# Kernel tuning notes

Hardware: AMD Instinct MI355X
Metric: run time of the kernel (lower is better)

Reference implementation:

```python
import jax, jax.numpy as jnp
import numpy as np

# ---- module config (init_kwargs) ----
B, CIN, H, W_ = 2, 64, 56, 56
COUT, KH, KW = 128, 3, 3
K = CIN * KH * KW               # 576, reduction dim
ARRAY_ROWS = 128
IN_SLICES = (2, 2, 2, 2)        # 8-bit inputs, 2-bit slices
W_SLICES = (2, 2, 2, 2)         # 8-bit weights, 2-bit slices
N_STEPS_IN = 2 ** sum(IN_SLICES)    # 256, unsigned quantizer
N_STEPS_W = 2 ** sum(W_SLICES)      # 256
ADC_BINS = 256
ADC_STEP = 4.0

def _shifts_masks(slices):
    masks, shifts = [], [0]
    for s in slices[::-1]:
        masks.append((1 << s) - 1)
        shifts.append(s + shifts[-1])
    return np.array(shifts[-2::-1], np.int32), np.array(masks[::-1], np.int32)

_ish, _im = _shifts_masks(IN_SLICES)
_wsh, _wm = _shifts_masks(W_SLICES)
ISH, IM = jnp.asarray(_ish), jnp.asarray(_im)
WSH, WM = jnp.asarray(_wsh), jnp.asarray(_wm)
ISF = jnp.asarray((1 << _ish).astype(np.float32))  # slice recombine weights 2^shift
WSF = jnp.asarray((1 << _wsh).astype(np.float32))


def setup_inputs() -> dict:
    key = jax.random.key(0)
    k1, k2 = jax.random.split(key)
    return {
        "x": jax.random.normal(k1, (B, CIN, H, W_), jnp.float32),
        "w": jax.random.normal(k2, (COUT, CIN, KH, KW), jnp.float32),
    }


def _im2col(x):
    # 3x3 SAME conv patches, ordering [Cin, kh, kw] to match w.reshape(COUT, K)
    xp = jnp.pad(x, ((0, 0), (0, 0), (1, 1), (1, 1)))
    cols = jnp.stack([xp[:, :, i:i + H, j:j + W_]
                      for i in range(KH) for j in range(KW)], axis=2)  # [B,Cin,9,H,W]
    return cols.transpose(0, 3, 4, 1, 2).reshape(B * H * W_, K)  # [Nx, K]


def _quant_unsigned(v, n_steps):
    # Quantizer.offset + Quantizer.forward (unsigned, per-row over dim=-1)
    offs = v.min(axis=-1, keepdims=True)
    vr = v - offs
    step = vr.max(axis=-1, keepdims=True) / (n_steps - 1)
    q = jnp.round(jnp.clip(vr, 0.0, step * n_steps) / step).astype(jnp.int32)
    return q, step[..., 0], offs[..., 0]


def _slice_bits(q, shifts, masks):
    # Slicer.forward: stack (q >> shift) & mask along new leading slice dim
    s = shifts.reshape((-1,) + (1,) * q.ndim)
    m = masks.reshape((-1,) + (1,) * q.ndim)
    return (q[None] >> s) & m


def _chunk(t):
    # Chunker.forward over last dim K
    nb = -(-K // ARRAY_ROWS)
    npb = -(-K // nb)
    pad = nb * npb - K
    t = jnp.pad(t, [(0, 0)] * (t.ndim - 1) + [(0, pad)])
    t = t.reshape(t.shape[:-1] + (nb, npb))
    return jnp.moveaxis(t, -2, 0)  # [nb, ..., npb]


def reference(x, w):
    xf = _im2col(x)                    # [Nx, K]
    wf = w.reshape(COUT, K)            # [Ny, K]
    x_sum = xf.sum(axis=-1)            # [Nx]
    w_sum = wf.sum(axis=-1)            # [Ny]

    xq, x_scale, x_offs = _quant_unsigned(xf, N_STEPS_IN)
    wq, w_scale, w_offs = _quant_unsigned(wf, N_STEPS_W)

    xc = _chunk(_slice_bits(xq, ISH, IM))  # [nb, nis, Nx, npb] int32
    wc = _chunk(_slice_bits(wq, WSH, WM))  # [nb, nws, Ny, npb] int32

    # bit-serial crossbar MACs per (chunk, weight-slice, input-slice)
    z = jnp.einsum('bixk,bwyk->bwixy',
                   xc.astype(jnp.float32), wc.astype(jnp.float32))  # [nb,nws,nis,Nx,Ny]

    # ADC digitization (unsigned, fixed step): quantize then dequantize
    z = jnp.round(jnp.clip(z, 0.0, ADC_STEP * ADC_BINS) / ADC_STEP) * ADC_STEP

    # Chunker.reverse: sum crossbar blocks; Slicer.reverse: shift-weighted sums
    z = z.sum(axis=0)                               # [nws,nis,Nx,Ny]
    z = jnp.einsum('wixy,w,i->xy', z, WSF, ISF)     # [Nx,Ny]

    # dequantize scales and unsigned-offset correction:
    # x.y = sx*sy*(xq.yq) + x_offs*sum(y) + y_offs*sum(x) - x_offs*y_offs*K
    z = z * x_scale[:, None] * w_scale[None, :]
    z = (z + x_offs[:, None] * w_sum[None, :]
           + w_offs[None, :] * x_sum[:, None]
           - x_offs[:, None] * w_offs[None, :] * K)

    return z.reshape(B, H, W_, COUT).transpose(0, 3, 1, 2)  # [B,Cout,H,W]
```

## Files before the change

kernel.cpp:

```cpp
#include <hip/hip_runtime.h>


#define NY    128
#define KDIM  576
#define NCH   5
#define NPB   116

typedef int i32x4 __attribute__((ext_vector_type(4)));
typedef float f32x4 __attribute__((ext_vector_type(4)));

extern __shared__ unsigned char lds[];

__device__ __forceinline__ i32x4 slice2b(i32x4 v, int sh) {
    i32x4 r;
    r[0] = (int)(((unsigned)v[0] >> sh) & 0x03030303u);
    r[1] = (int)(((unsigned)v[1] >> sh) & 0x03030303u);
    r[2] = (int)(((unsigned)v[2] >> sh) & 0x03030303u);
    r[3] = (int)(((unsigned)v[3] >> sh) & 0x03030303u);
    return r;
}

__device__ __forceinline__ void quant36(const float (&v)[36], unsigned char* rowp,
                                        int i16, float* sc_s, float* of_s,
                                        float* sm_s, int sidx)
{
    float mn = v[0], mx = v[0], sm = 0.f;
#pragma unroll
    for (int m = 0; m < 36; m++) { mn = fminf(mn, v[m]); mx = fmaxf(mx, v[m]); sm += v[m]; }
#pragma unroll
    for (int off = 1; off < 16; off <<= 1) {
        mn = fminf(mn, __shfl_xor(mn, off));
        mx = fmaxf(mx, __shfl_xor(mx, off));
        sm += __shfl_xor(sm, off);
    }
    float step = (mx - mn) / 255.0f;
    if (i16 == 0) { sc_s[sidx] = step; of_s[sidx] = mn; sm_s[sidx] = sm; }
    int k0 = i16 * 36;
#pragma unroll
    for (int d = 0; d < 9; d++) {
        unsigned int dw = 0;
#pragma unroll
        for (int mb = 0; mb < 4; mb++) {
            int q = (int)rintf((v[d * 4 + mb] - mn) / step);
            q = q < 0 ? 0 : (q > 255 ? 255 : q);
            dw |= (unsigned)q << (8 * mb);
        }
        int kd = k0 + d * 4;
        int ch = kd / NPB;
        *(unsigned int*)(rowp + kd + 12 * ch) = dw;
    }
}

__global__ __launch_bounds__(1024) void k_all(
    const float* __restrict__ x, const float* __restrict__ w,
    float* __restrict__ out)
{
    unsigned char* stgW = lds;
    unsigned char* stgX = lds + 81920;
    float* xsc = (float*)(lds + 102400);
    float* xof = xsc + 32;  float* xsm = xof + 32;
    float* wsc = xsm + 32;  float* wof = wsc + 128;  float* wsm = wof + 128;
    unsigned char* scr = lds + 104320;
    float* xs2 = (float*)(lds + 125312);

    int tid = threadIdx.x, wv = tid >> 6, lane = tid & 63;
    int g = lane >> 4, i16 = lane & 15;
    int blk = blockIdx.x;
    int b = blk >= 98 ? 1 : 0;
    int pos_base = (blk - 98 * b) * 32;
    const float* xb = x + (size_t)(b * 64) * 3136;

    for (int i = tid; i < 64 * 102; i += 1024) {
        int cin = i / 102, rem = i - cin * 102;
        int kh = rem / 34;
        int gg = pos_base + (rem - kh * 34) - 1;
        float vv = 0.f;
        if (gg >= 0 && gg < 3136) {
            int hg = gg / 56, wg = gg - hg * 56;
            int r = hg - 1 + kh;
            if (r >= 0 && r < 56) vv = xb[cin * 3136 + r * 56 + wg];
        }
        xs2[cin * 103 + rem] = vv;
    }
    if (tid < 512) {
        int tile = tid >> 8, rl = (tid >> 4) & 15, dwp = tid & 15;
        int col = dwp < 12 ? (dwp / 3) * 128 + 116 + (dwp % 3) * 4
                           : 624 + (dwp - 12) * 4;
        *(unsigned int*)(scr + tile * 10496 + rl * 656 + col) = 0u;
    }
    __syncthreads();

    if (wv < 8) {
        int i = wv * 4 + g;
        int pos = pos_base + i;
        int w_ = pos - (pos / 56) * 56;
        float v[36];
#pragma unroll
        for (int m = 0; m < 36; m++) {
            int r9 = m % 9, kh = r9 / 3, kw = r9 - kh * 3;
            int cin = i16 * 4 + m / 9;
            int ww = w_ - 1 + kw;
            v[m] = (ww >= 0 && ww < 56) ? xs2[cin * 103 + kh * 34 + i + kw] : 0.f;
        }
        quant36(v, scr + (i >> 4) * 10496 + (i & 15) * 656, i16, xsc, xof, xsm, i);
    }
    __syncthreads();

    for (int idx = tid; idx < 2 * 640; idx += 1024) {
        int tile = idx / 640, rr = idx - tile * 640;
        int u = rr >> 4, rl = rr & 15;
        *(i32x4*)(stgX + tile * 10240 + rr * 16) =
            *(const i32x4*)(scr + tile * 10496 + rl * 656 + u * 16);
    }
    __syncthreads();

    {
        int tile = tid >> 8, rl = (tid >> 4) & 15, dwp = tid & 15;
        int col = dwp < 12 ? (dwp / 3) * 128 + 116 + (dwp % 3) * 4
                           : 624 + (dwp - 12) * 4;
        *(unsigned int*)(scr + tile * 10496 + rl * 656 + col) = 0u;
    }
    {
        int row = wv * 4 + g;
        const float* wr = w + (size_t)row * KDIM + i16 * 36;
        float v[36];
#pragma unroll
        for (int d = 0; d < 9; d++) {
            f32x4 t = *(const f32x4*)(wr + d * 4);
            v[d*4+0] = t[0]; v[d*4+1] = t[1]; v[d*4+2] = t[2]; v[d*4+3] = t[3];
        }
        quant36(v, scr + (row >> 4) * 10496 + (row & 15) * 656, i16, wsc, wof, wsm, row);
    }
    __syncthreads();

    for (int idx = tid; idx < 4 * 640; idx += 1024) {
        int tile = idx / 640, rr = idx - tile * 640;
        int u = rr >> 4, rl = rr & 15;
        *(i32x4*)(stgW + tile * 10240 + rr * 16) =
            *(const i32x4*)(scr + tile * 10496 + rl * 656 + u * 16);
    }
    __syncthreads();

    {
        int row = 64 + wv * 4 + g;
        const float* wr = w + (size_t)row * KDIM + i16 * 36;
        float v[36];
#pragma unroll
        for (int d = 0; d < 9; d++) {
            f32x4 t = *(const f32x4*)(wr + d * 4);
            v[d*4+0] = t[0]; v[d*4+1] = t[1]; v[d*4+2] = t[2]; v[d*4+3] = t[3];
        }
        quant36(v, scr + ((row - 64) >> 4) * 10496 + (row & 15) * 656, i16, wsc, wof, wsm, row);
    }
    __syncthreads();

    for (int idx = tid; idx < 4 * 640; idx += 1024) {
        int tile = idx / 640, rr = idx - tile * 640;
        int u = rr >> 4, rl = rr & 15;
        *(i32x4*)(stgW + (4 + tile) * 10240 + rr * 16) =
            *(const i32x4*)(scr + tile * 10496 + rl * 656 + u * 16);
    }
    __syncthreads();

    int rt = wv >> 3, ctl = wv & 7;
    const unsigned char* Wb = stgW + ctl * 10240;
    const unsigned char* Xb = stgX + rt * 10240;

    i32x4 acc = {0, 0, 0, 0};
    const i32x4 zero = {0, 0, 0, 0};

    for (int chunk = 0; chunk < NCH; chunk++) {
        const i32x4* Ax = (const i32x4*)(Xb + chunk * 2048 + lane * 16);
        const i32x4* Aw = (const i32x4*)(Wb + chunk * 2048 + lane * 16);
        i32x4 ar0 = Ax[0], ar1 = Ax[64];
        i32x4 br0 = Aw[0], br1 = Aw[64];

        i32x4 ws_sl[4][2];
#pragma unroll
        for (int ws = 0; ws < 4; ws++) {
            ws_sl[ws][0] = slice2b(br0, 6 - 2 * ws);
            ws_sl[ws][1] = slice2b(br1, 6 - 2 * ws);
        }
#pragma unroll
        for (int is = 0; is < 4; is++) {
            int ish = 6 - 2 * is;
            i32x4 b0 = slice2b(ar0, ish);
            i32x4 b1 = slice2b(ar1, ish);
#pragma unroll
            for (int ws = 0; ws < 4; ws++) {
                i32x4 d = __builtin_amdgcn_mfma_i32_16x16x64_i8(ws_sl[ws][0], b0, zero, 0, 0, 0);
                d = __builtin_amdgcn_mfma_i32_16x16x64_i8(ws_sl[ws][1], b1, d, 0, 0, 0);
                int sh = ish + (6 - 2 * ws);
#pragma unroll
                for (int r = 0; r < 4; r++) {
                    int z = d[r];
                    z = z > 1024 ? 1024 : z;
                    int r4 = (z + 1 + ((z >> 2) & 1)) & ~3;
                    acc[r] += r4 << sh;
                }
            }
        }
    }

    int i_loc = rt * 16 + i16;
    float xs = xsc[i_loc], xo = xof[i_loc], xsmv = xsm[i_loc];
    int hw = pos_base + i_loc;
#pragma unroll
    for (int r = 0; r < 4; r++) {
        int wrow = ctl * 16 + g * 4 + r;
        float tt = ((float)acc[r] * xs) * wsc[wrow];
        float res = ((tt + xo * wsm[wrow]) + wof[wrow] * xsmv)
                  - (xo * wof[wrow]) * 576.0f;
        out[(b * 128 + wrow) * 3136 + hw] = res;
    }
}

extern "C" void kernel_launch(void* const* d_in, const int* in_sizes, int n_in,
                              void* d_out, int out_size, void* d_ws, size_t ws_size,
                              hipStream_t stream) {
    const float* x = (const float*)d_in[0];
    const float* w = (const float*)d_in[1];
    float* out = (float*)d_out;

    (void)hipFuncSetAttribute((const void*)k_all,
                              hipFuncAttributeMaxDynamicSharedMemorySize, 151680);

    hipLaunchKernelGGL(k_all, dim3(196), dim3(1024), 151680, stream, x, w, out);
}
```

Measured before the change: 41.19 us.

## Split weight quantization into separate kernel and shrink main tiles

Weight quantization moves out of every main-kernel block into a small prologue kernel that writes pre-quantized, MFMA-ordered weights plus their scales to workspace. The main kernel now uses 256-thread blocks over 16 positions and half of the output channels (784 blocks), and reads weight fragments straight from global memory. This removes the 196-fold redundant weight quantization and the large LDS footprint, raising occupancy. In exchange it adds a second launch and global-memory weight loads inside the MFMA loop, and recomputes the x halo tile twice per position tile.

```diff
diff --git a/kernel.cpp b/kernel.cpp
--- a/kernel.cpp
+++ b/kernel.cpp
@@ -1,15 +1,12 @@
 #include <hip/hip_runtime.h>
 
 
-#define NY    128
 #define KDIM  576
-#define NCH   5
 #define NPB   116
+#define SSTR  688
 
 typedef int i32x4 __attribute__((ext_vector_type(4)));
 typedef float f32x4 __attribute__((ext_vector_type(4)));
-
-extern __shared__ unsigned char lds[];
 
 __device__ __forceinline__ i32x4 slice2b(i32x4 v, int sh) {
     i32x4 r;
@@ -21,8 +18,8 @@
 }
 
 __device__ __forceinline__ void quant36(const float (&v)[36], unsigned char* rowp,
-                                        int i16, float* sc_s, float* of_s,
-                                        float* sm_s, int sidx)
+                                        int i16, float* sc, float* of,
+                                        float* sm_, int sidx)
 {
     float mn = v[0], mx = v[0], sm = 0.f;
 #pragma unroll
@@ -34,7 +31,7 @@
         sm += __shfl_xor(sm, off);
     }
     float step = (mx - mn) / 255.0f;
-    if (i16 == 0) { sc_s[sidx] = step; of_s[sidx] = mn; sm_s[sidx] = sm; }
+    if (i16 == 0) { sc[sidx] = step; of[sidx] = mn; sm_[sidx] = sm; }
     int k0 = i16 * 36;
 #pragma unroll
     for (int d = 0; d < 9; d++) {
@@ -51,48 +48,77 @@
     }
 }
 
-__global__ __launch_bounds__(1024) void k_all(
-    const float* __restrict__ x, const float* __restrict__ w,
-    float* __restrict__ out)
+__device__ __forceinline__ void zero_pads(unsigned char* scr, int tid) {
+    int rl = tid >> 4, dwp = tid & 15;
+    int col = dwp < 12 ? (dwp / 3) * 128 + 116 + (dwp % 3) * 4
+                       : 624 + (dwp - 12) * 4;
+    *(unsigned int*)(scr + rl * SSTR + col) = 0u;
+}
+
+__global__ __launch_bounds__(256) void k_wq(
+    const float* __restrict__ w, unsigned char* __restrict__ Wq,
+    float* __restrict__ wsc, float* __restrict__ wof, float* __restrict__ wsm)
 {
-    unsigned char* stgW = lds;
-    unsigned char* stgX = lds + 81920;
-    float* xsc = (float*)(lds + 102400);
-    float* xof = xsc + 32;  float* xsm = xof + 32;
-    float* wsc = xsm + 32;  float* wof = wsc + 128;  float* wsm = wof + 128;
-    unsigned char* scr = lds + 104320;
-    float* xs2 = (float*)(lds + 125312);
+    __shared__ __align__(16) unsigned char scrW[16 * SSTR];
+    int tid = threadIdx.x, wv = tid >> 6, lane = tid & 63;
+    int g = lane >> 4, i16 = lane & 15;
+    int ctile = blockIdx.x;
+
+    zero_pads(scrW, tid);
+    __syncthreads();
+
+    int rl = wv * 4 + g;
+    int row = ctile * 16 + rl;
+    const float* wr = w + (size_t)row * KDIM + i16 * 36;
+    float v[36];
+#pragma unroll
+    for (int d = 0; d < 9; d++) {
+        f32x4 t = *(const f32x4*)(wr + d * 4);
+        v[d*4+0] = t[0]; v[d*4+1] = t[1]; v[d*4+2] = t[2]; v[d*4+3] = t[3];
+    }
+    quant36(v, scrW + rl * SSTR, i16, wsc, wof, wsm, row);
+    __syncthreads();
+
+    for (int idx = tid; idx < 640; idx += 256)
+        *(i32x4*)(Wq + (size_t)ctile * 10240 + idx * 16) =
+            *(const i32x4*)(scrW + (idx & 15) * SSTR + (idx >> 4) * 16);
+}
+
+__global__ __launch_bounds__(256) void k_main(
+    const float* __restrict__ x, const unsigned char* __restrict__ Wq,
+    const float* __restrict__ wscg, const float* __restrict__ wofg,
+    const float* __restrict__ wsmg, float* __restrict__ out)
+{
+    __shared__ float xs2[64 * 57];
+    __shared__ __align__(16) unsigned char scrX[16 * SSTR];
+    __shared__ float xsc[16], xof[16], xsm[16];
 
     int tid = threadIdx.x, wv = tid >> 6, lane = tid & 63;
     int g = lane >> 4, i16 = lane & 15;
     int blk = blockIdx.x;
-    int b = blk >= 98 ? 1 : 0;
-    int pos_base = (blk - 98 * b) * 32;
+    int rtile = blk >> 1, chalf = blk & 1;
+    int b = rtile >= 196 ? 1 : 0;
+    int pos0 = (rtile - 196 * b) * 16;
     const float* xb = x + (size_t)(b * 64) * 3136;
 
-    for (int i = tid; i < 64 * 102; i += 1024) {
-        int cin = i / 102, rem = i - cin * 102;
-        int kh = rem / 34;
-        int gg = pos_base + (rem - kh * 34) - 1;
+    for (int i = tid; i < 64 * 54; i += 256) {
+        int cin = i / 54, rem = i - cin * 54;
+        int kh = rem / 18;
+        int gg = pos0 + (rem - kh * 18) - 1;
         float vv = 0.f;
         if (gg >= 0 && gg < 3136) {
             int hg = gg / 56, wg = gg - hg * 56;
             int r = hg - 1 + kh;
             if (r >= 0 && r < 56) vv = xb[cin * 3136 + r * 56 + wg];
         }
-        xs2[cin * 103 + rem] = vv;
-    }
-    if (tid < 512) {
-        int tile = tid >> 8, rl = (tid >> 4) & 15, dwp = tid & 15;
-        int col = dwp < 12 ? (dwp / 3) * 128 + 116 + (dwp % 3) * 4
-                           : 624 + (dwp - 12) * 4;
-        *(unsigned int*)(scr + tile * 10496 + rl * 656 + col) = 0u;
-    }
-    __syncthreads();
-
-    if (wv < 8) {
+        xs2[cin * 57 + rem] = vv;
+    }
+    zero_pads(scrX, tid);
+    __syncthreads();
+
+    {
         int i = wv * 4 + g;
-        int pos = pos_base + i;
+        int pos = pos0 + i;
         int w_ = pos - (pos / 56) * 56;
         float v[36];
 #pragma unroll
@@ -100,86 +126,30 @@
             int r9 = m % 9, kh = r9 / 3, kw = r9 - kh * 3;
             int cin = i16 * 4 + m / 9;
             int ww = w_ - 1 + kw;
-            v[m] = (ww >= 0 && ww < 56) ? xs2[cin * 103 + kh * 34 + i + kw] : 0.f;
-        }
-        quant36(v, scr + (i >> 4) * 10496 + (i & 15) * 656, i16, xsc, xof, xsm, i);
-    }
-    __syncthreads();
-
-    for (int idx = tid; idx < 2 * 640; idx += 1024) {
-        int tile = idx / 640, rr = idx - tile * 640;
-        int u = rr >> 4, rl = rr & 15;
-        *(i32x4*)(stgX + tile * 10240 + rr * 16) =
-            *(const i32x4*)(scr + tile * 10496 + rl * 656 + u * 16);
-    }
-    __syncthreads();
-
-    {
-        int tile = tid >> 8, rl = (tid >> 4) & 15, dwp = tid & 15;
-        int col = dwp < 12 ? (dwp / 3) * 128 + 116 + (dwp % 3) * 4
-                           : 624 + (dwp - 12) * 4;
-        *(unsigned int*)(scr + tile * 10496 + rl * 656 + col) = 0u;
-    }
-    {
-        int row = wv * 4 + g;
-        const float* wr = w + (size_t)row * KDIM + i16 * 36;
-        float v[36];
-#pragma unroll
-        for (int d = 0; d < 9; d++) {
-            f32x4 t = *(const f32x4*)(wr + d * 4);
-            v[d*4+0] = t[0]; v[d*4+1] = t[1]; v[d*4+2] = t[2]; v[d*4+3] = t[3];
-        }
-        quant36(v, scr + (row >> 4) * 10496 + (row & 15) * 656, i16, wsc, wof, wsm, row);
-    }
-    __syncthreads();
-
-    for (int idx = tid; idx < 4 * 640; idx += 1024) {
-        int tile = idx / 640, rr = idx - tile * 640;
-        int u = rr >> 4, rl = rr & 15;
-        *(i32x4*)(stgW + tile * 10240 + rr * 16) =
-            *(const i32x4*)(scr + tile * 10496 + rl * 656 + u * 16);
-    }
-    __syncthreads();
-
-    {
-        int row = 64 + wv * 4 + g;
-        const float* wr = w + (size_t)row * KDIM + i16 * 36;
-        float v[36];
-#pragma unroll
-        for (int d = 0; d < 9; d++) {
-            f32x4 t = *(const f32x4*)(wr + d * 4);
-            v[d*4+0] = t[0]; v[d*4+1] = t[1]; v[d*4+2] = t[2]; v[d*4+3] = t[3];
-        }
-        quant36(v, scr + ((row - 64) >> 4) * 10496 + (row & 15) * 656, i16, wsc, wof, wsm, row);
-    }
-    __syncthreads();
-
-    for (int idx = tid; idx < 4 * 640; idx += 1024) {
-        int tile = idx / 640, rr = idx - tile * 640;
-        int u = rr >> 4, rl = rr & 15;
-        *(i32x4*)(stgW + (4 + tile) * 10240 + rr * 16) =
-            *(const i32x4*)(scr + tile * 10496 + rl * 656 + u * 16);
-    }
-    __syncthreads();
-
-    int rt = wv >> 3, ctl = wv & 7;
-    const unsigned char* Wb = stgW + ctl * 10240;
-    const unsigned char* Xb = stgX + rt * 10240;
+            v[m] = (ww >= 0 && ww < 56) ? xs2[cin * 57 + kh * 18 + i + kw] : 0.f;
+        }
+        quant36(v, scrX + i * SSTR, i16, xsc, xof, xsm, i);
+    }
+    __syncthreads();
+
+    int ctl = chalf * 4 + wv;
+    const unsigned char* Wg = Wq + (size_t)ctl * 10240;
+    const unsigned char* xp = scrX + i16 * SSTR + g * 16;
 
     i32x4 acc = {0, 0, 0, 0};
     const i32x4 zero = {0, 0, 0, 0};
 
-    for (int chunk = 0; chunk < NCH; chunk++) {
-        const i32x4* Ax = (const i32x4*)(Xb + chunk * 2048 + lane * 16);
-        const i32x4* Aw = (const i32x4*)(Wb + chunk * 2048 + lane * 16);
-        i32x4 ar0 = Ax[0], ar1 = Ax[64];
-        i32x4 br0 = Aw[0], br1 = Aw[64];
-
-        i32x4 ws_sl[4][2];
+    for (int chunk = 0; chunk < 5; chunk++) {
+        i32x4 ar0 = *(const i32x4*)(xp + chunk * 128);
+        i32x4 ar1 = *(const i32x4*)(xp + chunk * 128 + 64);
+        const i32x4* Wp = (const i32x4*)(Wg + chunk * 2048) + lane;
+        i32x4 br0 = Wp[0], br1 = Wp[64];
+
+        i32x4 wsl[4][2];
 #pragma unroll
         for (int ws = 0; ws < 4; ws++) {
-            ws_sl[ws][0] = slice2b(br0, 6 - 2 * ws);
-            ws_sl[ws][1] = slice2b(br1, 6 - 2 * ws);
+            wsl[ws][0] = slice2b(br0, 6 - 2 * ws);
+            wsl[ws][1] = slice2b(br1, 6 - 2 * ws);
         }
 #pragma unroll
         for (int is = 0; is < 4; is++) {
@@ -188,8 +158,8 @@
             i32x4 b1 = slice2b(ar1, ish);
 #pragma unroll
             for (int ws = 0; ws < 4; ws++) {
-                i32x4 d = __builtin_amdgcn_mfma_i32_16x16x64_i8(ws_sl[ws][0], b0, zero, 0, 0, 0);
-                d = __builtin_amdgcn_mfma_i32_16x16x64_i8(ws_sl[ws][1], b1, d, 0, 0, 0);
+                i32x4 d = __builtin_amdgcn_mfma_i32_16x16x64_i8(wsl[ws][0], b0, zero, 0, 0, 0);
+                d = __builtin_amdgcn_mfma_i32_16x16x64_i8(wsl[ws][1], b1, d, 0, 0, 0);
                 int sh = ish + (6 - 2 * ws);
 #pragma unroll
                 for (int r = 0; r < 4; r++) {
@@ -202,16 +172,15 @@
         }
     }
 
-    int i_loc = rt * 16 + i16;
-    float xs = xsc[i_loc], xo = xof[i_loc], xsmv = xsm[i_loc];
-    int hw = pos_base + i_loc;
+    float xs = xsc[i16], xo = xof[i16], xsmv = xsm[i16];
+    int hw = pos0 + i16;
 #pragma unroll
     for (int r = 0; r < 4; r++) {
         int wrow = ctl * 16 + g * 4 + r;
-        float tt = ((float)acc[r] * xs) * wsc[wrow];
-        float res = ((tt + xo * wsm[wrow]) + wof[wrow] * xsmv)
-                  - (xo * wof[wrow]) * 576.0f;
-        out[(b * 128 + wrow) * 3136 + hw] = res;
+        float tt = ((float)acc[r] * xs) * wscg[wrow];
+        float res = ((tt + xo * wsmg[wrow]) + wofg[wrow] * xsmv)
+                  - (xo * wofg[wrow]) * 576.0f;
+        out[(size_t)(b * 128 + wrow) * 3136 + hw] = res;
     }
 }
 
@@ -222,8 +191,12 @@
     const float* w = (const float*)d_in[1];
     float* out = (float*)d_out;
 
-    (void)hipFuncSetAttribute((const void*)k_all,
-                              hipFuncAttributeMaxDynamicSharedMemorySize, 151680);
-
-    hipLaunchKernelGGL(k_all, dim3(196), dim3(1024), 151680, stream, x, w, out);
-}
+    unsigned char* Wq = (unsigned char*)d_ws;
+    float* wsc = (float*)(Wq + 81920);
+    float* wof = wsc + 128;
+    float* wsm = wof + 128;
+
+    hipLaunchKernelGGL(k_wq, dim3(8), dim3(256), 0, stream, w, Wq, wsc, wof, wsm);
+    hipLaunchKernelGGL(k_main, dim3(784), dim3(256), 0, stream,
+                       x, Wq, wsc, wof, wsm, out);
+}
```

Result: faster. 40.00 us (-2.9%).
